# Kernel tuning notes

Measured on AMD Instinct MI355X. Metric: run time of the kernel, lower is better.

Reference implementation:

```python
import jax, jax.numpy as jnp
import numpy as np

D_MODEL = 512
MAX_LEN = 1024
N_BATCH = 128
N_PART = 512


def make_encoding(d_model, max_len):
    pos = np.arange(max_len, dtype=np.float32)[:, None]            # [L,1]
    _2i = np.arange(0, d_model, 2, dtype=np.float32)[None, :]      # [1,D/2]
    angle = pos / np.power(10000.0, _2i / d_model)                 # [L,D/2]
    enc = np.zeros((max_len, d_model), dtype=np.float32)
    enc[:, 0::2] = np.sin(angle)
    enc[:, 1::2] = np.cos(angle)
    return jnp.asarray(enc)


def setup_inputs() -> dict:
    key = jax.random.key(0)
    k1, k2, k3, k4, k5 = jax.random.split(key, 5)
    dfn = jax.random.randint(k1, (N_BATCH, N_PART), 0, MAX_LEN, dtype=jnp.int64)
    dfn_fa = jax.random.randint(k2, (N_BATCH, N_PART), 0, MAX_LEN, dtype=jnp.int64)
    latent = jax.random.normal(k3, (N_BATCH, N_PART, D_MODEL), dtype=jnp.float32)
    # Linear(2*d_model -> d_model), torch default init scale ~1/sqrt(fan_in)
    bound = 1.0 / np.sqrt(2 * D_MODEL)
    W = jax.random.uniform(k4, (2 * D_MODEL, D_MODEL), jnp.float32, -bound, bound)
    b = jax.random.uniform(k5, (D_MODEL,), jnp.float32, -bound, bound)
    encoding = make_encoding(D_MODEL, MAX_LEN)
    return {"dfn": dfn, "dfn_fa": dfn_fa, "tokenized_parts_latent": latent,
            "encoding": encoding, "W": W, "b": b}


def reference(dfn, dfn_fa, tokenized_parts_latent, encoding, W, b):
    # gather position embeddings for node and parent DFS numbers, add
    pos_emb = encoding[dfn] + encoding[dfn_fa]                     # [B,P,D]
    x = jnp.concatenate([pos_emb, tokenized_parts_latent], axis=-1)  # [B,P,2D]
    out = jnp.einsum('bpk,kd->bpd', x, W) + b                      # [B,P,D]
    return out
```

## Files before the change

kernel.cpp:

```cpp
#include <hip/hip_runtime.h>
#include <hip/hip_bf16.h>
#include <stdint.h>

typedef float f32x4 __attribute__((ext_vector_type(4)));
typedef short short8 __attribute__((ext_vector_type(8)));
typedef __bf16 bf16x8 __attribute__((ext_vector_type(8)));

#define D_MODEL 512
#define MAX_LEN 1024
#define M_TOTAL 65536

static __device__ __forceinline__ short f2bf(float f) {
  union { __hip_bfloat16 h; short s; } u;
  u.h = __float2bfloat16(f);
  return u.s;
}

static __device__ __forceinline__ bf16x8 as_bf16x8(short8 s) {
  union { short8 s; bf16x8 b; } u;
  u.s = s;
  return u.b;
}

static __device__ __forceinline__ void gload_lds16(const void* g, void* l) {
  __builtin_amdgcn_global_load_lds(
      (const __attribute__((address_space(1))) uint32_t*)(uintptr_t)g,
      (__attribute__((address_space(3))) uint32_t*)(uint32_t)(uintptr_t)l,
      16, 0, 0);
}

static __device__ __forceinline__ void mfma_bf16(f32x4& c, short8 a, short8 b) {
  asm("v_mfma_f32_16x16x32_bf16 %0, %1, %2, %0" : "+v"(c) : "v"(a), "v"(b));
}

__global__ __launch_bounds__(256) void prep_w_kernel(const float* __restrict__ W,
                                                     short* __restrict__ WtT,
                                                     short* __restrict__ WbT) {
  __shared__ float tile[64][65];
  const int t = threadIdx.x;
  const int nt = blockIdx.x * 64;
  const int kt = blockIdx.y * 64;
  const int c = t & 63;
  const int r0 = t >> 6;
#pragma unroll
  for (int r = r0; r < 64; r += 4)
    tile[r][c] = W[(size_t)(kt + r) * D_MODEL + nt + c];
  __syncthreads();
  short* dst = (kt < D_MODEL) ? WtT : WbT;
  const int kb = kt & (D_MODEL - 1);
#pragma unroll
  for (int n = r0; n < 64; n += 4)
    dst[(size_t)(nt + n) * D_MODEL + kb + c] = f2bf(tile[c][n]);
}

__global__ __launch_bounds__(256) void prep_enc_kernel(const float* __restrict__ enc,
                                                       short* __restrict__ encb) {
  const int i = (blockIdx.x * 256 + threadIdx.x) * 4;
  float4 v = *reinterpret_cast<const float4*>(enc + i);
  short4 r = make_short4(f2bf(v.x), f2bf(v.y), f2bf(v.z), f2bf(v.w));
  *reinterpret_cast<short4*>(encb + i) = r;
}

__global__ __launch_bounds__(256) void gemm_encw_kernel(const short* __restrict__ A,
                                                        const short* __restrict__ BT,
                                                        float* __restrict__ C) {
  __shared__ short As[128 * 32];
  __shared__ short Bs[128 * 32];
  const int t = threadIdx.x;
  const int lane = t & 63;
  const int wave = t >> 6;
  const int wm = wave >> 1, wn = wave & 1;
  const int m0 = blockIdx.y * 128, n0 = blockIdx.x * 128;
  const int koff = (t & 3) * 8;
  const int rr = t >> 2;
  const int l15 = lane & 15, lk = (lane >> 4) * 8;
  f32x4 acc[4][4] = {};
  for (int kt = 0; kt < D_MODEL; kt += 32) {
    __syncthreads();
    gload_lds16(A + (size_t)(m0 + rr) * D_MODEL + kt + koff, (char*)As + t * 16);
    gload_lds16(A + (size_t)(m0 + 64 + rr) * D_MODEL + kt + koff, (char*)As + 4096 + t * 16);
    gload_lds16(BT + (size_t)(n0 + rr) * D_MODEL + kt + koff, (char*)Bs + t * 16);
    gload_lds16(BT + (size_t)(n0 + 64 + rr) * D_MODEL + kt + koff, (char*)Bs + 4096 + t * 16);
    __syncthreads();
    short8 af[4], bfr[4];
#pragma unroll
    for (int mi = 0; mi < 4; ++mi)
      af[mi] = *reinterpret_cast<const short8*>(&As[(wm * 64 + mi * 16 + l15) * 32 + lk]);
#pragma unroll
    for (int ni = 0; ni < 4; ++ni)
      bfr[ni] = *reinterpret_cast<const short8*>(&Bs[(wn * 64 + ni * 16 + l15) * 32 + lk]);
#pragma unroll
    for (int mi = 0; mi < 4; ++mi)
#pragma unroll
      for (int ni = 0; ni < 4; ++ni)
        mfma_bf16(acc[mi][ni], af[mi], bfr[ni]);
  }
#pragma unroll
  for (int mi = 0; mi < 4; ++mi)
#pragma unroll
    for (int r = 0; r < 4; ++r) {
      const int row = m0 + wm * 64 + mi * 16 + (lane >> 4) * 4 + r;
#pragma unroll
      for (int ni = 0; ni < 4; ++ni) {
        const int col = n0 + wn * 64 + ni * 16 + l15;
        C[(size_t)row * D_MODEL + col] = acc[mi][ni][r];
      }
    }
}

__global__ __launch_bounds__(256, 4) void gemm_main_kernel(
    const float* __restrict__ latent,
    const short* __restrict__ BT,
    const float* __restrict__ encW,
    const int* __restrict__ dfn,
    const int* __restrict__ dfa,
    const float* __restrict__ bias,
    float* __restrict__ out) {
  __shared__ alignas(16) float Af[128 * 32];
  __shared__ alignas(16) short Bs[128 * 32];
  const int t = threadIdx.x;
  const int lane = t & 63;
  const int wave = t >> 6;
  const int wm = wave >> 1, wn = wave & 1;

  const int bid = blockIdx.x;
  const int slot = bid >> 3;
  const int mblk = (bid & 7) * 64 + (slot >> 2);
  const int nblk = slot & 3;
  const int m0 = mblk * 128, n0 = nblk * 128;

  const int l15 = lane & 15;
  const int lsl = lane >> 4;

  const int arow = t >> 3;
  const int acol = ((t & 7) ^ (arow & 7)) * 4;
  const float* aSrc[4];
#pragma unroll
  for (int p = 0; p < 4; ++p)
    aSrc[p] = latent + (size_t)(m0 + p * 32 + arow) * D_MODEL + acol;

  const int brow = t >> 2;
  const int bcol = ((t & 3) ^ ((t >> 3) & 3)) * 8;
  const short* bSrc[2];
#pragma unroll
  for (int p = 0; p < 2; ++p)
    bSrc[p] = BT + (size_t)(n0 + p * 64 + brow) * D_MODEL + bcol;

  f32x4 acc[4][4] = {};

  for (int kt = 0; kt < D_MODEL; kt += 32) {
    __syncthreads();
#pragma unroll
    for (int p = 0; p < 4; ++p)
      gload_lds16(aSrc[p] + kt, (char*)Af + p * 4096 + t * 16);
#pragma unroll
    for (int p = 0; p < 2; ++p)
      gload_lds16(bSrc[p] + kt, (char*)Bs + p * 4096 + t * 16);
    __syncthreads();
    bf16x8 af[4], bfv[4];
#pragma unroll
    for (int mi = 0; mi < 4; ++mi) {
      const int r = wm * 64 + mi * 16 + l15;
      const int s0 = (2 * lsl) ^ (r & 7);
      const int s1 = (2 * lsl + 1) ^ (r & 7);
      f32x4 v0 = *reinterpret_cast<const f32x4*>((const char*)Af + r * 128 + s0 * 16);
      f32x4 v1 = *reinterpret_cast<const f32x4*>((const char*)Af + r * 128 + s1 * 16);
      short8 h;
      h[0] = f2bf(v0[0]); h[1] = f2bf(v0[1]); h[2] = f2bf(v0[2]); h[3] = f2bf(v0[3]);
      h[4] = f2bf(v1[0]); h[5] = f2bf(v1[1]); h[6] = f2bf(v1[2]); h[7] = f2bf(v1[3]);
      af[mi] = as_bf16x8(h);
    }
#pragma unroll
    for (int ni = 0; ni < 4; ++ni) {
      const int r = wn * 64 + ni * 16 + l15;
      const int s = lsl ^ ((r >> 1) & 3);
      bfv[ni] = as_bf16x8(
          *reinterpret_cast<const short8*>((const char*)Bs + r * 64 + s * 16));
    }
#pragma unroll
    for (int mi = 0; mi < 4; ++mi)
#pragma unroll
      for (int ni = 0; ni < 4; ++ni)
        acc[mi][ni] = __builtin_amdgcn_mfma_f32_16x16x32_bf16(
            af[mi], bfv[ni], acc[mi][ni], 0, 0, 0);
  }

#pragma unroll
  for (int mi = 0; mi < 4; ++mi) {
#pragma unroll
    for (int r = 0; r < 4; ++r) {
      const int row = m0 + wm * 64 + mi * 16 + lsl * 4 + r;
      const int d1 = dfn[row];
      const int d2 = dfa[row];
      const float* e1 = encW + (size_t)d1 * D_MODEL;
      const float* e2 = encW + (size_t)d2 * D_MODEL;
      const size_t ro = (size_t)row * D_MODEL;
#pragma unroll
      for (int ni = 0; ni < 4; ++ni) {
        const int col = n0 + wn * 64 + ni * 16 + l15;
        out[ro + col] = acc[mi][ni][r] + e1[col] + e2[col] + bias[col];
      }
    }
  }
}

extern "C" void kernel_launch(void* const* d_in, const int* in_sizes, int n_in,
                              void* d_out, int out_size, void* d_ws, size_t ws_size,
                              hipStream_t stream) {
  const int* dfn = (const int*)d_in[0];
  const int* dfa = (const int*)d_in[1];
  const float* latent = (const float*)d_in[2];
  const float* enc = (const float*)d_in[3];
  const float* W = (const float*)d_in[4];
  const float* bias = (const float*)d_in[5];
  float* out = (float*)d_out;

  char* ws = (char*)d_ws;
  short* WtT  = (short*)(ws);
  short* WbT  = (short*)(ws + 512 * 1024);
  short* encb = (short*)(ws + 1024 * 1024);
  float* encW = (float*)(ws + 2 * 1024 * 1024);

  hipLaunchKernelGGL(prep_w_kernel, dim3(8, 16), dim3(256), 0, stream, W, WtT, WbT);
  hipLaunchKernelGGL(prep_enc_kernel, dim3(512), dim3(256), 0, stream, enc, encb);
  hipLaunchKernelGGL(gemm_encw_kernel, dim3(4, 8), dim3(256), 0, stream, encb, WtT, encW);
  hipLaunchKernelGGL(gemm_main_kernel, dim3(2048), dim3(256), 0, stream,
                     latent, WbT, encW, dfn, dfa, bias, out);
}
```

Baseline: 115.9 us.

## Pre-gather positional term into bf16 buffer and double K-tile depth

Adds a separate kernel that gathers the two projected encoding rows per token plus bias, sums them and stores a bf16 M×D buffer, so the GEMM epilogue reads one contiguous bf16 value instead of three scattered fp32 loads. It also doubles the main GEMM's K step from 32 to 64, halving the number of barrier pairs, and lowers the occupancy hint to 3 because of the larger shared tiles. The cost is an extra 64 MB write and 64 MB read of intermediate traffic, bf16 rounding of the positional term, and a path that depends on workspace size.

```diff
diff --git a/kernel.cpp b/kernel.cpp
--- a/kernel.cpp
+++ b/kernel.cpp
@@ -14,6 +14,12 @@
   union { __hip_bfloat16 h; short s; } u;
   u.h = __float2bfloat16(f);
   return u.s;
+}
+
+static __device__ __forceinline__ float bf2f(unsigned short u) {
+  union { unsigned int i; float f; } v;
+  v.i = ((unsigned int)u) << 16;
+  return v.f;
 }
 
 static __device__ __forceinline__ bf16x8 as_bf16x8(short8 s) {
@@ -108,16 +114,46 @@
     }
 }
 
-__global__ __launch_bounds__(256, 4) void gemm_main_kernel(
+__global__ __launch_bounds__(256) void gather_pos_kernel(
+    const float* __restrict__ encW, const int* __restrict__ dfn,
+    const int* __restrict__ dfa, const float* __restrict__ bias,
+    unsigned short* __restrict__ posW) {
+  const int t = threadIdx.x;
+  const int row = blockIdx.x * 32 + (t >> 3);
+  const int c0 = (t & 7) * 64;
+  const float* e1 = encW + (size_t)dfn[row] * D_MODEL + c0;
+  const float* e2 = encW + (size_t)dfa[row] * D_MODEL + c0;
+  const float* bi = bias + c0;
+  unsigned short* dst = posW + (size_t)row * D_MODEL + c0;
+#pragma unroll
+  for (int c = 0; c < 8; ++c) {
+    f32x4 a0 = *reinterpret_cast<const f32x4*>(e1 + c * 8);
+    f32x4 a1 = *reinterpret_cast<const f32x4*>(e1 + c * 8 + 4);
+    f32x4 b0 = *reinterpret_cast<const f32x4*>(e2 + c * 8);
+    f32x4 b1 = *reinterpret_cast<const f32x4*>(e2 + c * 8 + 4);
+    f32x4 s0 = *reinterpret_cast<const f32x4*>(bi + c * 8);
+    f32x4 s1 = *reinterpret_cast<const f32x4*>(bi + c * 8 + 4);
+    short8 h;
+    h[0] = f2bf(a0[0] + b0[0] + s0[0]); h[1] = f2bf(a0[1] + b0[1] + s0[1]);
+    h[2] = f2bf(a0[2] + b0[2] + s0[2]); h[3] = f2bf(a0[3] + b0[3] + s0[3]);
+    h[4] = f2bf(a1[0] + b1[0] + s1[0]); h[5] = f2bf(a1[1] + b1[1] + s1[1]);
+    h[6] = f2bf(a1[2] + b1[2] + s1[2]); h[7] = f2bf(a1[3] + b1[3] + s1[3]);
+    *reinterpret_cast<short8*>(dst + c * 8) = h;
+  }
+}
+
+__global__ __launch_bounds__(256, 3) void gemm_main_kernel(
     const float* __restrict__ latent,
     const short* __restrict__ BT,
     const float* __restrict__ encW,
     const int* __restrict__ dfn,
     const int* __restrict__ dfa,
     const float* __restrict__ bias,
+    const unsigned short* __restrict__ posW,
+    int use_pos,
     float* __restrict__ out) {
-  __shared__ alignas(16) float Af[128 * 32];
-  __shared__ alignas(16) short Bs[128 * 32];
+  __shared__ alignas(16) float Af[128 * 64];
+  __shared__ alignas(16) short Bs[128 * 64];
   const int t = threadIdx.x;
   const int lane = t & 63;
   const int wave = t >> 6;
@@ -132,73 +168,83 @@
   const int l15 = lane & 15;
   const int lsl = lane >> 4;
 
-  const int arow = t >> 3;
-  const int acol = ((t & 7) ^ (arow & 7)) * 4;
-  const float* aSrc[4];
-#pragma unroll
-  for (int p = 0; p < 4; ++p)
-    aSrc[p] = latent + (size_t)(m0 + p * 32 + arow) * D_MODEL + acol;
-
-  const int brow = t >> 2;
-  const int bcol = ((t & 3) ^ ((t >> 3) & 3)) * 8;
-  const short* bSrc[2];
-#pragma unroll
-  for (int p = 0; p < 2; ++p)
-    bSrc[p] = BT + (size_t)(n0 + p * 64 + brow) * D_MODEL + bcol;
+  const int arow = t >> 4;
+  const float* aSrc = latent + (size_t)(m0 + arow) * D_MODEL + ((t & 15) ^ arow) * 4;
+  const int brow = t >> 3;
+  const short* bSrc = BT + (size_t)(n0 + brow) * D_MODEL + ((t & 7) ^ (brow & 7)) * 8;
 
   f32x4 acc[4][4] = {};
 
-  for (int kt = 0; kt < D_MODEL; kt += 32) {
-    __syncthreads();
+  for (int kt = 0; kt < D_MODEL; kt += 64) {
+    __syncthreads();
+#pragma unroll
+    for (int p = 0; p < 8; ++p)
+      gload_lds16(aSrc + (size_t)p * 16 * D_MODEL + kt, (char*)Af + p * 4096 + t * 16);
 #pragma unroll
     for (int p = 0; p < 4; ++p)
-      gload_lds16(aSrc[p] + kt, (char*)Af + p * 4096 + t * 16);
-#pragma unroll
-    for (int p = 0; p < 2; ++p)
-      gload_lds16(bSrc[p] + kt, (char*)Bs + p * 4096 + t * 16);
-    __syncthreads();
-    bf16x8 af[4], bfv[4];
+      gload_lds16(bSrc + (size_t)p * 32 * D_MODEL + kt, (char*)Bs + p * 4096 + t * 16);
+    __syncthreads();
+#pragma unroll
+    for (int kk = 0; kk < 2; ++kk) {
+      bf16x8 af[4], bfv[4];
+#pragma unroll
+      for (int mi = 0; mi < 4; ++mi) {
+        const int r = wm * 64 + mi * 16 + l15;
+        const int s0 = (kk * 8 + lsl * 2) ^ (r & 15);
+        const int s1 = (kk * 8 + lsl * 2 + 1) ^ (r & 15);
+        f32x4 v0 = *reinterpret_cast<const f32x4*>((const char*)Af + r * 256 + s0 * 16);
+        f32x4 v1 = *reinterpret_cast<const f32x4*>((const char*)Af + r * 256 + s1 * 16);
+        short8 h;
+        h[0] = f2bf(v0[0]); h[1] = f2bf(v0[1]); h[2] = f2bf(v0[2]); h[3] = f2bf(v0[3]);
+        h[4] = f2bf(v1[0]); h[5] = f2bf(v1[1]); h[6] = f2bf(v1[2]); h[7] = f2bf(v1[3]);
+        af[mi] = as_bf16x8(h);
+      }
+#pragma unroll
+      for (int ni = 0; ni < 4; ++ni) {
+        const int r = wn * 64 + ni * 16 + l15;
+        const int s = (kk * 4 + lsl) ^ (r & 7);
+        bfv[ni] = as_bf16x8(
+            *reinterpret_cast<const short8*>((const char*)Bs + r * 128 + s * 16));
+      }
+#pragma unroll
+      for (int mi = 0; mi < 4; ++mi)
+#pragma unroll
+        for (int ni = 0; ni < 4; ++ni)
+          acc[mi][ni] = __builtin_amdgcn_mfma_f32_16x16x32_bf16(
+              af[mi], bfv[ni], acc[mi][ni], 0, 0, 0);
+    }
+  }
+
+  if (use_pos) {
 #pragma unroll
     for (int mi = 0; mi < 4; ++mi) {
-      const int r = wm * 64 + mi * 16 + l15;
-      const int s0 = (2 * lsl) ^ (r & 7);
-      const int s1 = (2 * lsl + 1) ^ (r & 7);
-      f32x4 v0 = *reinterpret_cast<const f32x4*>((const char*)Af + r * 128 + s0 * 16);
-      f32x4 v1 = *reinterpret_cast<const f32x4*>((const char*)Af + r * 128 + s1 * 16);
-      short8 h;
-      h[0] = f2bf(v0[0]); h[1] = f2bf(v0[1]); h[2] = f2bf(v0[2]); h[3] = f2bf(v0[3]);
-      h[4] = f2bf(v1[0]); h[5] = f2bf(v1[1]); h[6] = f2bf(v1[2]); h[7] = f2bf(v1[3]);
-      af[mi] = as_bf16x8(h);
-    }
-#pragma unroll
-    for (int ni = 0; ni < 4; ++ni) {
-      const int r = wn * 64 + ni * 16 + l15;
-      const int s = lsl ^ ((r >> 1) & 3);
-      bfv[ni] = as_bf16x8(
-          *reinterpret_cast<const short8*>((const char*)Bs + r * 64 + s * 16));
-    }
-#pragma unroll
-    for (int mi = 0; mi < 4; ++mi)
-#pragma unroll
-      for (int ni = 0; ni < 4; ++ni)
-        acc[mi][ni] = __builtin_amdgcn_mfma_f32_16x16x32_bf16(
-            af[mi], bfv[ni], acc[mi][ni], 0, 0, 0);
-  }
-
-#pragma unroll
-  for (int mi = 0; mi < 4; ++mi) {
-#pragma unroll
-    for (int r = 0; r < 4; ++r) {
-      const int row = m0 + wm * 64 + mi * 16 + lsl * 4 + r;
-      const int d1 = dfn[row];
-      const int d2 = dfa[row];
-      const float* e1 = encW + (size_t)d1 * D_MODEL;
-      const float* e2 = encW + (size_t)d2 * D_MODEL;
-      const size_t ro = (size_t)row * D_MODEL;
-#pragma unroll
-      for (int ni = 0; ni < 4; ++ni) {
-        const int col = n0 + wn * 64 + ni * 16 + l15;
-        out[ro + col] = acc[mi][ni][r] + e1[col] + e2[col] + bias[col];
+#pragma unroll
+      for (int r = 0; r < 4; ++r) {
+        const int row = m0 + wm * 64 + mi * 16 + lsl * 4 + r;
+        const size_t ro = (size_t)row * D_MODEL;
+#pragma unroll
+        for (int ni = 0; ni < 4; ++ni) {
+          const int col = n0 + wn * 64 + ni * 16 + l15;
+          out[ro + col] = acc[mi][ni][r] + bf2f(posW[ro + col]);
+        }
+      }
+    }
+  } else {
+#pragma unroll
+    for (int mi = 0; mi < 4; ++mi) {
+#pragma unroll
+      for (int r = 0; r < 4; ++r) {
+        const int row = m0 + wm * 64 + mi * 16 + lsl * 4 + r;
+        const int d1 = dfn[row];
+        const int d2 = dfa[row];
+        const float* e1 = encW + (size_t)d1 * D_MODEL;
+        const float* e2 = encW + (size_t)d2 * D_MODEL;
+        const size_t ro = (size_t)row * D_MODEL;
+#pragma unroll
+        for (int ni = 0; ni < 4; ++ni) {
+          const int col = n0 + wn * 64 + ni * 16 + l15;
+          out[ro + col] = acc[mi][ni][r] + e1[col] + e2[col] + bias[col];
+        }
       }
     }
   }
@@ -220,10 +266,17 @@
   short* WbT  = (short*)(ws + 512 * 1024);
   short* encb = (short*)(ws + 1024 * 1024);
   float* encW = (float*)(ws + 2 * 1024 * 1024);
+  const size_t POSW_OFF = 4u * 1024 * 1024;
+  unsigned short* posW = (unsigned short*)(ws + POSW_OFF);
+  const size_t need = POSW_OFF + (size_t)M_TOTAL * D_MODEL * 2;
+  const int use_pos = (ws_size >= need) ? 1 : 0;
 
   hipLaunchKernelGGL(prep_w_kernel, dim3(8, 16), dim3(256), 0, stream, W, WtT, WbT);
   hipLaunchKernelGGL(prep_enc_kernel, dim3(512), dim3(256), 0, stream, enc, encb);
   hipLaunchKernelGGL(gemm_encw_kernel, dim3(4, 8), dim3(256), 0, stream, encb, WtT, encW);
+  if (use_pos)
+    hipLaunchKernelGGL(gather_pos_kernel, dim3(2048), dim3(256), 0, stream,
+                       encW, dfn, dfa, bias, posW);
   hipLaunchKernelGGL(gemm_main_kernel, dim3(2048), dim3(256), 0, stream,
-                     latent, WbT, encW, dfn, dfa, bias, out);
-}
+                     latent, WbT, encW, dfn, dfa, bias, posW, use_pos, out);
+}
```

Result: slower. 177.6 us (+53.2%).
